# Optimization experiments

Hardware: AMD Instinct MI355X
Metric: run time of the kernel (lower is better)

## Reference

```python
import jax, jax.numpy as jnp
import numpy as np

NUM_SYM = 50000
NUM_HERB = 50000
N_NODES = NUM_SYM + NUM_HERB
DIM = 128
N_EDGES = 3200000
N_LAYERS = 2


def setup_inputs() -> dict:
    key = jax.random.key(0)
    k1, k2, k3, k4, k5 = jax.random.split(key, 5)
    sym_emb = jax.random.normal(k1, (NUM_SYM, DIM), dtype=jnp.float32)
    herb_emb = jax.random.normal(k2, (NUM_HERB, DIM), dtype=jnp.float32)
    adj_rows = jax.random.randint(k3, (N_EDGES,), 0, N_NODES, dtype=jnp.int32)
    adj_cols = jax.random.randint(k4, (N_EDGES,), 0, N_NODES, dtype=jnp.int32)
    # normalized-Laplacian values are positive; uniform stands in for D^-1/2 A D^-1/2 entries
    adj_vals = jax.random.uniform(k5, (N_EDGES,), dtype=jnp.float32)
    return {"sym_emb": sym_emb, "herb_emb": herb_emb,
            "adj_rows": adj_rows, "adj_cols": adj_cols, "adj_vals": adj_vals}


def _spmm(rows, cols, vals, x):
    # sparse [N,N] @ dense [N,D]: gather source rows, scale, scatter-add to dest rows
    msgs = vals[:, None] * x[cols]              # [E, D]
    return jax.ops.segment_sum(msgs, rows, num_segments=N_NODES)


def reference(sym_emb, herb_emb, adj_rows, adj_cols, adj_vals):
    ego = jnp.concatenate([sym_emb, herb_emb], axis=0)   # [N, D]
    acc = ego
    e = ego
    for _ in range(N_LAYERS):
        e = _spmm(adj_rows, adj_cols, adj_vals, e)
        acc = acc + e
    all_emb = acc / jnp.float32(N_LAYERS + 1)            # mean over stacked layers
    return all_emb[:NUM_SYM], all_emb[NUM_SYM:]
```

## Files before the change

kernel.cpp:

```cpp
#include <hip/hip_runtime.h>

#define NUM_SYM 50000
#define NUM_HERB 50000
#define N_NODES (NUM_SYM + NUM_HERB)
#define DIM 128
#define NB_BUCKETS ((N_NODES + 255) / 256)
#define CHUNK 8192
#define PAD 16

__device__ __forceinline__ float bf2f(unsigned short u) {
    return __uint_as_float((unsigned)u << 16);
}
__device__ __forceinline__ unsigned short f2bf(float f) {
    unsigned u = __float_as_uint(f);
    unsigned r = (u + 0x7FFFu + ((u >> 16) & 1u)) >> 16;
    return (unsigned short)r;
}

__global__ __launch_bounds__(256) void to_bf16(
    const float* __restrict__ sym, const float* __restrict__ herb,
    ushort* __restrict__ xbf)
{
    int i = blockIdx.x * 256 + threadIdx.x;
    const int n4 = N_NODES * DIM / 4;
    if (i >= n4) return;
    const int sym4 = NUM_SYM * DIM / 4;
    float4 v = (i < sym4) ? reinterpret_cast<const float4*>(sym)[i]
                          : reinterpret_cast<const float4*>(herb)[i - sym4];
    ushort4 o;
    o.x = f2bf(v.x); o.y = f2bf(v.y); o.z = f2bf(v.z); o.w = f2bf(v.w);
    reinterpret_cast<ushort4*>(xbf)[i] = o;
}


__global__ __launch_bounds__(256) void hist_buckets(
    const int* __restrict__ rows, int E, int* __restrict__ bucket_cnt)
{
    __shared__ int h[NB_BUCKETS];
    for (int i = threadIdx.x; i < NB_BUCKETS; i += 256) h[i] = 0;
    __syncthreads();
    int start = blockIdx.x * CHUNK;
    int end   = min(start + CHUNK, E);
    for (int e = start + threadIdx.x; e < end; e += 256)
        atomicAdd(&h[rows[e] >> 8], 1);
    __syncthreads();
    for (int i = threadIdx.x; i < NB_BUCKETS; i += 256)
        if (h[i]) atomicAdd(&bucket_cnt[i * PAD], h[i]);
}

__global__ __launch_bounds__(512) void scan_buckets(
    const int* __restrict__ cnt, int* __restrict__ off, int* __restrict__ cursor)
{
    __shared__ int s[512];
    int t = threadIdx.x;
    int v = (t < NB_BUCKETS) ? cnt[t * PAD] : 0;
    s[t] = v;
    __syncthreads();
    for (int o = 1; o < 512; o <<= 1) {
        int x = (t >= o) ? s[t - o] : 0;
        __syncthreads();
        s[t] += x;
        __syncthreads();
    }
    if (t < NB_BUCKETS) { off[t] = s[t] - v; cursor[t * PAD] = s[t] - v; }
    if (t == NB_BUCKETS - 1) off[NB_BUCKETS] = s[t];
}

__global__ __launch_bounds__(256) void scatter_buckets(
    const int* __restrict__ rows, const int* __restrict__ cols,
    const float* __restrict__ vals, int E,
    int* __restrict__ cursor, int2* __restrict__ bucketed)
{
    __shared__ int lh[NB_BUCKETS];
    __shared__ int lbase[NB_BUCKETS];
    for (int i = threadIdx.x; i < NB_BUCKETS; i += 256) lh[i] = 0;
    __syncthreads();
    int start = blockIdx.x * CHUNK;
    int end   = min(start + CHUNK, E);
    for (int e = start + threadIdx.x; e < end; e += 256)
        atomicAdd(&lh[rows[e] >> 8], 1);
    __syncthreads();
    for (int i = threadIdx.x; i < NB_BUCKETS; i += 256) {
        int c = lh[i];
        lbase[i] = c ? atomicAdd(&cursor[i * PAD], c) : 0;
        lh[i] = 0;
    }
    __syncthreads();
    for (int e = start + threadIdx.x; e < end; e += 256) {
        int r = rows[e];
        int key = r >> 8;
        int pos = lbase[key] + atomicAdd(&lh[key], 1);
        bucketed[pos] = make_int2(((r & 255) << 17) | cols[e],
                                  __float_as_int(vals[e]));
    }
}

__global__ __launch_bounds__(512) void bucket_to_csr(
    const int2* __restrict__ bucketed, const int* __restrict__ off,
    int* __restrict__ csr, int* __restrict__ rowptr)
{
    __shared__ int h[256];
    int b = blockIdx.x, t = threadIdx.x;
    int s0 = off[b], s1 = off[b + 1];
    if (t < 256) h[t] = 0;
    __syncthreads();
    for (int j = s0 + t; j < s1; j += 512)
        atomicAdd(&h[(unsigned)bucketed[j].x >> 17], 1);
    __syncthreads();
    int v = (t < 256) ? h[t] : 0;
    for (int o = 1; o < 256; o <<= 1) {
        int x = (t < 256 && t >= o) ? h[t - o] : 0;
        __syncthreads();
        if (t < 256) h[t] += x;
        __syncthreads();
    }
    if (t < 256) {
        int r = b * 256 + t;
        if (r < N_NODES) rowptr[r] = s0 + (h[t] - v);
    }
    __syncthreads();
    if (t < 256) h[t] -= v;
    __syncthreads();
    for (int j = s0 + t; j < s1; j += 512) {
        int2 rec = bucketed[j];
        int key = (unsigned)rec.x >> 17;
        int pos = s0 + atomicAdd(&h[key], 1);
        unsigned vb = (unsigned)f2bf(__int_as_float(rec.y));
        csr[pos] = (int)((vb << 17) | ((unsigned)rec.x & 0x1FFFFu));
    }
}

__device__ __forceinline__ float unpack_val(int p) {
    return __uint_as_float(((unsigned)p >> 17) << 16);
}

template <bool FUSE_MEAN>
__global__ __launch_bounds__(256) void spmm_csr_bf16(
    const int* __restrict__ csr, const int* __restrict__ rowptr, int E,
    const ushort* __restrict__ xbf,
    const float* __restrict__ sym, const float* __restrict__ herb,
    const ushort* __restrict__ e1bf,
    void* __restrict__ outp)
{
    int wave = blockIdx.x * 4 + (threadIdx.x >> 6);
    int half = (threadIdx.x >> 5) & 1;
    int lane = threadIdx.x & 31;
    int r = wave * 2 + half;
    if (r >= N_NODES) return;

    int j   = rowptr[r];
    int end = (r + 1 < N_NODES) ? rowptr[r + 1] : E;

    float4 acc = make_float4(0.f, 0.f, 0.f, 0.f);
    for (; j + 3 < end; j += 4) {
        int p0 = csr[j], p1 = csr[j + 1], p2 = csr[j + 2], p3 = csr[j + 3];
        ushort4 m0 = reinterpret_cast<const ushort4*>(xbf + (size_t)(p0 & 0x1FFFF) * DIM)[lane];
        ushort4 m1 = reinterpret_cast<const ushort4*>(xbf + (size_t)(p1 & 0x1FFFF) * DIM)[lane];
        ushort4 m2 = reinterpret_cast<const ushort4*>(xbf + (size_t)(p2 & 0x1FFFF) * DIM)[lane];
        ushort4 m3 = reinterpret_cast<const ushort4*>(xbf + (size_t)(p3 & 0x1FFFF) * DIM)[lane];
        float v0 = unpack_val(p0), v1 = unpack_val(p1);
        float v2 = unpack_val(p2), v3 = unpack_val(p3);
        acc.x += v0 * bf2f(m0.x) + v1 * bf2f(m1.x) + v2 * bf2f(m2.x) + v3 * bf2f(m3.x);
        acc.y += v0 * bf2f(m0.y) + v1 * bf2f(m1.y) + v2 * bf2f(m2.y) + v3 * bf2f(m3.y);
        acc.z += v0 * bf2f(m0.z) + v1 * bf2f(m1.z) + v2 * bf2f(m2.z) + v3 * bf2f(m3.z);
        acc.w += v0 * bf2f(m0.w) + v1 * bf2f(m1.w) + v2 * bf2f(m2.w) + v3 * bf2f(m3.w);
    }
    for (; j < end; ++j) {
        int p0 = csr[j];
        float v0 = unpack_val(p0);
        ushort4 m0 = reinterpret_cast<const ushort4*>(xbf + (size_t)(p0 & 0x1FFFF) * DIM)[lane];
        acc.x += v0 * bf2f(m0.x);
        acc.y += v0 * bf2f(m0.y);
        acc.z += v0 * bf2f(m0.z);
        acc.w += v0 * bf2f(m0.w);
    }

    if (FUSE_MEAN) {
        const float4* egorow = (r < NUM_SYM)
            ? reinterpret_cast<const float4*>(sym  + (size_t)r * DIM)
            : reinterpret_cast<const float4*>(herb + (size_t)(r - NUM_SYM) * DIM);
        float4 g = egorow[lane];
        ushort4 a = reinterpret_cast<const ushort4*>(e1bf + (size_t)r * DIM)[lane];
        const float s = 1.0f / 3.0f;
        acc.x = (g.x + bf2f(a.x) + acc.x) * s;
        acc.y = (g.y + bf2f(a.y) + acc.y) * s;
        acc.z = (g.z + bf2f(a.z) + acc.z) * s;
        acc.w = (g.w + bf2f(a.w) + acc.w) * s;
        reinterpret_cast<float4*>((float*)outp + (size_t)r * DIM)[lane] = acc;
    } else {
        ushort4 o;
        o.x = f2bf(acc.x); o.y = f2bf(acc.y); o.z = f2bf(acc.z); o.w = f2bf(acc.w);
        reinterpret_cast<ushort4*>((ushort*)outp + (size_t)r * DIM)[lane] = o;
    }
}

__global__ __launch_bounds__(256) void spmm_scatter(
    const int* __restrict__ rows, const int* __restrict__ cols,
    const float* __restrict__ vals, int n_edges,
    const float* __restrict__ xa, const float* __restrict__ xb,
    float* __restrict__ out)
{
    int gid = blockIdx.x * 256 + threadIdx.x;
    int edge = gid >> 5;
    if (edge >= n_edges) return;
    int sub = gid & 31;
    int c = cols[edge];
    int r = rows[edge];
    float v = vals[edge];
    const float* xrow = (c < NUM_SYM) ? (xa + (size_t)c * DIM)
                                      : (xb + (size_t)(c - NUM_SYM) * DIM);
    float4 m = reinterpret_cast<const float4*>(xrow)[sub];
    float* o = out + (size_t)r * DIM + (size_t)sub * 4;
    unsafeAtomicAdd(o + 0, v * m.x);
    unsafeAtomicAdd(o + 1, v * m.y);
    unsafeAtomicAdd(o + 2, v * m.z);
    unsafeAtomicAdd(o + 3, v * m.w);
}

__global__ __launch_bounds__(256) void finalize_mean(
    const float* __restrict__ sym, const float* __restrict__ herb,
    const float* __restrict__ e1, float* __restrict__ out)
{
    int i = blockIdx.x * 256 + threadIdx.x;
    const int n4 = N_NODES * DIM / 4;
    if (i >= n4) return;
    const int sym4 = NUM_SYM * DIM / 4;
    float4 e = (i < sym4) ? reinterpret_cast<const float4*>(sym)[i]
                          : reinterpret_cast<const float4*>(herb)[i - sym4];
    float4 a = reinterpret_cast<const float4*>(e1)[i];
    float4 b = reinterpret_cast<float4*>(out)[i];
    const float s = 1.0f / 3.0f;
    float4 r;
    r.x = (e.x + a.x + b.x) * s;
    r.y = (e.y + a.y + b.y) * s;
    r.z = (e.z + a.z + b.z) * s;
    r.w = (e.w + a.w + b.w) * s;
    reinterpret_cast<float4*>(out)[i] = r;
}

extern "C" void kernel_launch(void* const* d_in, const int* in_sizes, int n_in,
                              void* d_out, int out_size, void* d_ws, size_t ws_size,
                              hipStream_t stream) {
    const float* sym  = (const float*)d_in[0];
    const float* herb = (const float*)d_in[1];
    const int*   rows = (const int*)d_in[2];
    const int*   cols = (const int*)d_in[3];
    const float* vals = (const float*)d_in[4];
    const int E = in_sizes[2];
    float* out = (float*)d_out;

    char* ws = (char*)d_ws;
    auto align256 = [](size_t x) { return (x + 255) & ~(size_t)255; };
    const size_t xbf_bytes   = (size_t)N_NODES * DIM * sizeof(ushort);
    const size_t csr_off     = align256(xbf_bytes);
    const size_t buck_off    = align256(csr_off + (size_t)E * 4);
    const size_t buck_bytes  = (size_t)E * 8 > xbf_bytes ? (size_t)E * 8 : xbf_bytes;
    const size_t rowptr_off  = align256(buck_off + buck_bytes);
    const size_t bcnt_off    = align256(rowptr_off + (size_t)N_NODES * 4);
    const size_t boff_off    = align256(bcnt_off + (size_t)NB_BUCKETS * PAD * 4);
    const size_t bcur_off    = align256(boff_off + (size_t)(NB_BUCKETS + 1) * 4);
    const size_t required    = bcur_off + (size_t)NB_BUCKETS * PAD * 4;

    if (ws_size < required || E >= (1 << 22)) {
        float* e1 = (float*)ws;
        const size_t e1_bytes = (size_t)N_NODES * DIM * sizeof(float);
        hipMemsetAsync(e1, 0, e1_bytes, stream);
        hipMemsetAsync(out, 0, e1_bytes, stream);
        const int spmm_blocks = (E * 32 + 255) / 256;
        spmm_scatter<<<spmm_blocks, 256, 0, stream>>>(rows, cols, vals, E, sym, herb, e1);
        spmm_scatter<<<spmm_blocks, 256, 0, stream>>>(rows, cols, vals, E,
                                                      e1, e1 + (size_t)NUM_SYM * DIM, out);
        const int n4 = N_NODES * DIM / 4;
        finalize_mean<<<(n4 + 255) / 256, 256, 0, stream>>>(sym, herb, e1, out);
        return;
    }

    ushort* xbf      = (ushort*)ws;
    int*    csr      = (int*)(ws + csr_off);
    int2*   bucketed = (int2*)(ws + buck_off);
    ushort* e1bf     = (ushort*)(ws + buck_off);
    int*    rowptr   = (int*)(ws + rowptr_off);
    int*    bcnt     = (int*)(ws + bcnt_off);
    int*    boff     = (int*)(ws + boff_off);
    int*    bcur     = (int*)(ws + bcur_off);

    hipMemsetAsync(bcnt, 0, (size_t)NB_BUCKETS * PAD * 4, stream);
    const int EB = (E + CHUNK - 1) / CHUNK;
    hist_buckets<<<EB, 256, 0, stream>>>(rows, E, bcnt);
    scan_buckets<<<1, 512, 0, stream>>>(bcnt, boff, bcur);
    scatter_buckets<<<EB, 256, 0, stream>>>(rows, cols, vals, E, bcur, bucketed);
    bucket_to_csr<<<NB_BUCKETS, 512, 0, stream>>>(bucketed, boff, csr, rowptr);

    const int n4 = N_NODES * DIM / 4;
    to_bf16<<<(n4 + 255) / 256, 256, 0, stream>>>(sym, herb, xbf);

    const int blocks = (N_NODES / 2 + 3) / 4;
    spmm_csr_bf16<false><<<blocks, 256, 0, stream>>>(csr, rowptr, E, xbf,
                                                     nullptr, nullptr, nullptr, e1bf);
    spmm_csr_bf16<true><<<blocks, 256, 0, stream>>>(csr, rowptr, E, e1bf,
                                                    sym, herb, e1bf, out);
}
```

Baseline: 474.1 us.

## Build CSR with direct per-row atomics and unroll SpMM gather by eight

Replaces the four-kernel bucketed sort with a three-step CSR build: a global per-row atomic histogram, a single-block segmented scan that writes rowptr and cursors, and an atomic scatter straight into packed CSR. This drops the intermediate 8-byte bucketed record pass and two kernels. The cost is millions of contended global atomics with return and scattered 4-byte writes. The SpMM inner loop is unrolled to eight edges to expose more memory-level parallelism, and CSR loads and the final output store use nontemporal hints.

```diff
diff --git a/kernel.cpp b/kernel.cpp
--- a/kernel.cpp
+++ b/kernel.cpp
@@ -4,9 +4,8 @@
 #define NUM_HERB 50000
 #define N_NODES (NUM_SYM + NUM_HERB)
 #define DIM 128
-#define NB_BUCKETS ((N_NODES + 255) / 256)
-#define CHUNK 8192
-#define PAD 16
+
+typedef float floatx4 __attribute__((ext_vector_type(4)));
 
 __device__ __forceinline__ float bf2f(unsigned short u) {
     return __uint_as_float((unsigned)u << 16);
@@ -32,101 +31,69 @@
     reinterpret_cast<ushort4*>(xbf)[i] = o;
 }
 
-
-__global__ __launch_bounds__(256) void hist_buckets(
-    const int* __restrict__ rows, int E, int* __restrict__ bucket_cnt)
-{
-    __shared__ int h[NB_BUCKETS];
-    for (int i = threadIdx.x; i < NB_BUCKETS; i += 256) h[i] = 0;
+__global__ __launch_bounds__(256) void hist_rows(
+    const int* __restrict__ rows, int E, int* __restrict__ cnt)
+{
+    int stride = gridDim.x * 256;
+    for (int e = blockIdx.x * 256 + threadIdx.x; e < E; e += stride)
+        atomicAdd(&cnt[rows[e]], 1);
+}
+
+#define SEG 100
+__global__ __launch_bounds__(1024) void scan_rows(
+    const int* __restrict__ cnt, int* __restrict__ rowptr, int* __restrict__ cursor)
+{
+    __shared__ int s[1024];
+    int t = threadIdx.x;
+    int base = t * SEG;
+    int sum = 0;
+    if (base < N_NODES) {
+        const int4* c4 = reinterpret_cast<const int4*>(cnt + base);
+        #pragma unroll
+        for (int i = 0; i < SEG / 4; ++i) {
+            int4 v = c4[i];
+            sum += v.x + v.y + v.z + v.w;
+        }
+    }
+    s[t] = sum;
     __syncthreads();
-    int start = blockIdx.x * CHUNK;
-    int end   = min(start + CHUNK, E);
-    for (int e = start + threadIdx.x; e < end; e += 256)
-        atomicAdd(&h[rows[e] >> 8], 1);
-    __syncthreads();
-    for (int i = threadIdx.x; i < NB_BUCKETS; i += 256)
-        if (h[i]) atomicAdd(&bucket_cnt[i * PAD], h[i]);
-}
-
-__global__ __launch_bounds__(512) void scan_buckets(
-    const int* __restrict__ cnt, int* __restrict__ off, int* __restrict__ cursor)
-{
-    __shared__ int s[512];
-    int t = threadIdx.x;
-    int v = (t < NB_BUCKETS) ? cnt[t * PAD] : 0;
-    s[t] = v;
-    __syncthreads();
-    for (int o = 1; o < 512; o <<= 1) {
+    for (int o = 1; o < 1024; o <<= 1) {
         int x = (t >= o) ? s[t - o] : 0;
         __syncthreads();
         s[t] += x;
         __syncthreads();
     }
-    if (t < NB_BUCKETS) { off[t] = s[t] - v; cursor[t * PAD] = s[t] - v; }
-    if (t == NB_BUCKETS - 1) off[NB_BUCKETS] = s[t];
-}
-
-__global__ __launch_bounds__(256) void scatter_buckets(
+    int run = s[t] - sum;
+    if (base < N_NODES) {
+        const int4* c4 = reinterpret_cast<const int4*>(cnt + base);
+        int4* rp4 = reinterpret_cast<int4*>(rowptr + base);
+        int4* cu4 = reinterpret_cast<int4*>(cursor + base);
+        #pragma unroll
+        for (int i = 0; i < SEG / 4; ++i) {
+            int4 v = c4[i];
+            int4 o4;
+            o4.x = run;
+            o4.y = o4.x + v.x;
+            o4.z = o4.y + v.y;
+            o4.w = o4.z + v.z;
+            run  = o4.w + v.w;
+            rp4[i] = o4;
+            cu4[i] = o4;
+        }
+    }
+}
+
+__global__ __launch_bounds__(256) void scatter_csr(
     const int* __restrict__ rows, const int* __restrict__ cols,
     const float* __restrict__ vals, int E,
-    int* __restrict__ cursor, int2* __restrict__ bucketed)
-{
-    __shared__ int lh[NB_BUCKETS];
-    __shared__ int lbase[NB_BUCKETS];
-    for (int i = threadIdx.x; i < NB_BUCKETS; i += 256) lh[i] = 0;
-    __syncthreads();
-    int start = blockIdx.x * CHUNK;
-    int end   = min(start + CHUNK, E);
-    for (int e = start + threadIdx.x; e < end; e += 256)
-        atomicAdd(&lh[rows[e] >> 8], 1);
-    __syncthreads();
-    for (int i = threadIdx.x; i < NB_BUCKETS; i += 256) {
-        int c = lh[i];
-        lbase[i] = c ? atomicAdd(&cursor[i * PAD], c) : 0;
-        lh[i] = 0;
-    }
-    __syncthreads();
-    for (int e = start + threadIdx.x; e < end; e += 256) {
+    int* __restrict__ cursor, int* __restrict__ csr)
+{
+    int stride = gridDim.x * 256;
+    for (int e = blockIdx.x * 256 + threadIdx.x; e < E; e += stride) {
         int r = rows[e];
-        int key = r >> 8;
-        int pos = lbase[key] + atomicAdd(&lh[key], 1);
-        bucketed[pos] = make_int2(((r & 255) << 17) | cols[e],
-                                  __float_as_int(vals[e]));
-    }
-}
-
-__global__ __launch_bounds__(512) void bucket_to_csr(
-    const int2* __restrict__ bucketed, const int* __restrict__ off,
-    int* __restrict__ csr, int* __restrict__ rowptr)
-{
-    __shared__ int h[256];
-    int b = blockIdx.x, t = threadIdx.x;
-    int s0 = off[b], s1 = off[b + 1];
-    if (t < 256) h[t] = 0;
-    __syncthreads();
-    for (int j = s0 + t; j < s1; j += 512)
-        atomicAdd(&h[(unsigned)bucketed[j].x >> 17], 1);
-    __syncthreads();
-    int v = (t < 256) ? h[t] : 0;
-    for (int o = 1; o < 256; o <<= 1) {
-        int x = (t < 256 && t >= o) ? h[t - o] : 0;
-        __syncthreads();
-        if (t < 256) h[t] += x;
-        __syncthreads();
-    }
-    if (t < 256) {
-        int r = b * 256 + t;
-        if (r < N_NODES) rowptr[r] = s0 + (h[t] - v);
-    }
-    __syncthreads();
-    if (t < 256) h[t] -= v;
-    __syncthreads();
-    for (int j = s0 + t; j < s1; j += 512) {
-        int2 rec = bucketed[j];
-        int key = (unsigned)rec.x >> 17;
-        int pos = s0 + atomicAdd(&h[key], 1);
-        unsigned vb = (unsigned)f2bf(__int_as_float(rec.y));
-        csr[pos] = (int)((vb << 17) | ((unsigned)rec.x & 0x1FFFFu));
+        int pos = atomicAdd(&cursor[r], 1);
+        unsigned vb = (unsigned)f2bf(vals[e]);
+        csr[pos] = (int)((vb << 17) | (unsigned)cols[e]);
     }
 }
 
@@ -152,8 +119,41 @@
     int end = (r + 1 < N_NODES) ? rowptr[r + 1] : E;
 
     float4 acc = make_float4(0.f, 0.f, 0.f, 0.f);
+    for (; j + 7 < end; j += 8) {
+        int p0 = __builtin_nontemporal_load(csr + j);
+        int p1 = __builtin_nontemporal_load(csr + j + 1);
+        int p2 = __builtin_nontemporal_load(csr + j + 2);
+        int p3 = __builtin_nontemporal_load(csr + j + 3);
+        int p4 = __builtin_nontemporal_load(csr + j + 4);
+        int p5 = __builtin_nontemporal_load(csr + j + 5);
+        int p6 = __builtin_nontemporal_load(csr + j + 6);
+        int p7 = __builtin_nontemporal_load(csr + j + 7);
+        ushort4 m0 = reinterpret_cast<const ushort4*>(xbf + (size_t)(p0 & 0x1FFFF) * DIM)[lane];
+        ushort4 m1 = reinterpret_cast<const ushort4*>(xbf + (size_t)(p1 & 0x1FFFF) * DIM)[lane];
+        ushort4 m2 = reinterpret_cast<const ushort4*>(xbf + (size_t)(p2 & 0x1FFFF) * DIM)[lane];
+        ushort4 m3 = reinterpret_cast<const ushort4*>(xbf + (size_t)(p3 & 0x1FFFF) * DIM)[lane];
+        ushort4 m4 = reinterpret_cast<const ushort4*>(xbf + (size_t)(p4 & 0x1FFFF) * DIM)[lane];
+        ushort4 m5 = reinterpret_cast<const ushort4*>(xbf + (size_t)(p5 & 0x1FFFF) * DIM)[lane];
+        ushort4 m6 = reinterpret_cast<const ushort4*>(xbf + (size_t)(p6 & 0x1FFFF) * DIM)[lane];
+        ushort4 m7 = reinterpret_cast<const ushort4*>(xbf + (size_t)(p7 & 0x1FFFF) * DIM)[lane];
+        float v0 = unpack_val(p0), v1 = unpack_val(p1);
+        float v2 = unpack_val(p2), v3 = unpack_val(p3);
+        float v4 = unpack_val(p4), v5 = unpack_val(p5);
+        float v6 = unpack_val(p6), v7 = unpack_val(p7);
+        acc.x += v0 * bf2f(m0.x) + v1 * bf2f(m1.x) + v2 * bf2f(m2.x) + v3 * bf2f(m3.x)
+               + v4 * bf2f(m4.x) + v5 * bf2f(m5.x) + v6 * bf2f(m6.x) + v7 * bf2f(m7.x);
+        acc.y += v0 * bf2f(m0.y) + v1 * bf2f(m1.y) + v2 * bf2f(m2.y) + v3 * bf2f(m3.y)
+               + v4 * bf2f(m4.y) + v5 * bf2f(m5.y) + v6 * bf2f(m6.y) + v7 * bf2f(m7.y);
+        acc.z += v0 * bf2f(m0.z) + v1 * bf2f(m1.z) + v2 * bf2f(m2.z) + v3 * bf2f(m3.z)
+               + v4 * bf2f(m4.z) + v5 * bf2f(m5.z) + v6 * bf2f(m6.z) + v7 * bf2f(m7.z);
+        acc.w += v0 * bf2f(m0.w) + v1 * bf2f(m1.w) + v2 * bf2f(m2.w) + v3 * bf2f(m3.w)
+               + v4 * bf2f(m4.w) + v5 * bf2f(m5.w) + v6 * bf2f(m6.w) + v7 * bf2f(m7.w);
+    }
     for (; j + 3 < end; j += 4) {
-        int p0 = csr[j], p1 = csr[j + 1], p2 = csr[j + 2], p3 = csr[j + 3];
+        int p0 = __builtin_nontemporal_load(csr + j);
+        int p1 = __builtin_nontemporal_load(csr + j + 1);
+        int p2 = __builtin_nontemporal_load(csr + j + 2);
+        int p3 = __builtin_nontemporal_load(csr + j + 3);
         ushort4 m0 = reinterpret_cast<const ushort4*>(xbf + (size_t)(p0 & 0x1FFFF) * DIM)[lane];
         ushort4 m1 = reinterpret_cast<const ushort4*>(xbf + (size_t)(p1 & 0x1FFFF) * DIM)[lane];
         ushort4 m2 = reinterpret_cast<const ushort4*>(xbf + (size_t)(p2 & 0x1FFFF) * DIM)[lane];
@@ -166,7 +166,7 @@
         acc.w += v0 * bf2f(m0.w) + v1 * bf2f(m1.w) + v2 * bf2f(m2.w) + v3 * bf2f(m3.w);
     }
     for (; j < end; ++j) {
-        int p0 = csr[j];
+        int p0 = __builtin_nontemporal_load(csr + j);
         float v0 = unpack_val(p0);
         ushort4 m0 = reinterpret_cast<const ushort4*>(xbf + (size_t)(p0 & 0x1FFFF) * DIM)[lane];
         acc.x += v0 * bf2f(m0.x);
@@ -182,11 +182,13 @@
         float4 g = egorow[lane];
         ushort4 a = reinterpret_cast<const ushort4*>(e1bf + (size_t)r * DIM)[lane];
         const float s = 1.0f / 3.0f;
-        acc.x = (g.x + bf2f(a.x) + acc.x) * s;
-        acc.y = (g.y + bf2f(a.y) + acc.y) * s;
-        acc.z = (g.z + bf2f(a.z) + acc.z) * s;
-        acc.w = (g.w + bf2f(a.w) + acc.w) * s;
-        reinterpret_cast<float4*>((float*)outp + (size_t)r * DIM)[lane] = acc;
+        floatx4 o;
+        o.x = (g.x + bf2f(a.x) + acc.x) * s;
+        o.y = (g.y + bf2f(a.y) + acc.y) * s;
+        o.z = (g.z + bf2f(a.z) + acc.z) * s;
+        o.w = (g.w + bf2f(a.w) + acc.w) * s;
+        __builtin_nontemporal_store(o,
+            reinterpret_cast<floatx4*>((float*)outp + (size_t)r * DIM) + lane);
     } else {
         ushort4 o;
         o.x = f2bf(acc.x); o.y = f2bf(acc.y); o.z = f2bf(acc.z); o.w = f2bf(acc.w);
@@ -253,13 +255,9 @@
     auto align256 = [](size_t x) { return (x + 255) & ~(size_t)255; };
     const size_t xbf_bytes   = (size_t)N_NODES * DIM * sizeof(ushort);
     const size_t csr_off     = align256(xbf_bytes);
-    const size_t buck_off    = align256(csr_off + (size_t)E * 4);
-    const size_t buck_bytes  = (size_t)E * 8 > xbf_bytes ? (size_t)E * 8 : xbf_bytes;
-    const size_t rowptr_off  = align256(buck_off + buck_bytes);
-    const size_t bcnt_off    = align256(rowptr_off + (size_t)N_NODES * 4);
-    const size_t boff_off    = align256(bcnt_off + (size_t)NB_BUCKETS * PAD * 4);
-    const size_t bcur_off    = align256(boff_off + (size_t)(NB_BUCKETS + 1) * 4);
-    const size_t required    = bcur_off + (size_t)NB_BUCKETS * PAD * 4;
+    const size_t e1_off      = align256(csr_off + (size_t)E * 4);
+    const size_t rowptr_off  = align256(e1_off + xbf_bytes);
+    const size_t required    = rowptr_off + (size_t)N_NODES * 4;
 
     if (ws_size < required || E >= (1 << 22)) {
         float* e1 = (float*)ws;
@@ -275,21 +273,17 @@
         return;
     }
 
-    ushort* xbf      = (ushort*)ws;
-    int*    csr      = (int*)(ws + csr_off);
-    int2*   bucketed = (int2*)(ws + buck_off);
-    ushort* e1bf     = (ushort*)(ws + buck_off);
-    int*    rowptr   = (int*)(ws + rowptr_off);
-    int*    bcnt     = (int*)(ws + bcnt_off);
-    int*    boff     = (int*)(ws + boff_off);
-    int*    bcur     = (int*)(ws + bcur_off);
-
-    hipMemsetAsync(bcnt, 0, (size_t)NB_BUCKETS * PAD * 4, stream);
-    const int EB = (E + CHUNK - 1) / CHUNK;
-    hist_buckets<<<EB, 256, 0, stream>>>(rows, E, bcnt);
-    scan_buckets<<<1, 512, 0, stream>>>(bcnt, boff, bcur);
-    scatter_buckets<<<EB, 256, 0, stream>>>(rows, cols, vals, E, bcur, bucketed);
-    bucket_to_csr<<<NB_BUCKETS, 512, 0, stream>>>(bucketed, boff, csr, rowptr);
+    ushort* xbf    = (ushort*)ws;
+    int*    cursor = (int*)ws;
+    int*    csr    = (int*)(ws + csr_off);
+    int*    cnt    = (int*)(ws + csr_off);
+    ushort* e1bf   = (ushort*)(ws + e1_off);
+    int*    rowptr = (int*)(ws + rowptr_off);
+
+    hipMemsetAsync(cnt, 0, (size_t)N_NODES * 4, stream);
+    hist_rows<<<2048, 256, 0, stream>>>(rows, E, cnt);
+    scan_rows<<<1, 1024, 0, stream>>>(cnt, rowptr, cursor);
+    scatter_csr<<<2048, 256, 0, stream>>>(rows, cols, vals, E, cursor, csr);
 
     const int n4 = N_NODES * DIM / 4;
     to_bf16<<<(n4 + 255) / 256, 256, 0, stream>>>(sym, herb, xbf);
```

New measurement: 787.8 us. +66.2%, slower.
